# Optimization experiments

Hardware: AMD Instinct MI355X
Metric: run time of the kernel (lower is better)

## Reference

```python
import jax, jax.numpy as jnp
import numpy as np

N_NODES = 1_000_000
N_EDGES = 32_000_000
N_GRAPHS = 1024
N_LAYERS = 8


def setup_inputs() -> dict:
    key = jax.random.key(0)
    k1, k2, k3, k4, k5, k6, k7 = jax.random.split(key, 7)
    x = jnp.ones((N_NODES, 1), dtype=jnp.float32)
    src = jax.random.randint(k1, (N_EDGES,), 0, N_NODES, dtype=jnp.int32)
    dst = jax.random.randint(k2, (N_EDGES,), 0, N_NODES, dtype=jnp.int32)
    edge_weight = jax.random.uniform(k3, (N_EDGES,), dtype=jnp.float32)
    graph_ids = jnp.sort(jax.random.randint(k4, (N_NODES,), 0, N_GRAPHS, dtype=jnp.int32))
    W_neigh = jax.random.normal(k5, (N_LAYERS, 1, 1), dtype=jnp.float32)
    b_neigh = jax.random.normal(k6, (N_LAYERS, 1), dtype=jnp.float32)
    W_self = jax.random.normal(k7, (N_LAYERS, 1, 1), dtype=jnp.float32)
    return {"x": x, "src": src, "dst": dst, "edge_weight": edge_weight,
            "graph_ids": graph_ids, "W_neigh": W_neigh, "b_neigh": b_neigh,
            "W_self": W_self}


def reference(x, src, dst, edge_weight, graph_ids, W_neigh, b_neigh, W_self):
    # FixedNet forward with conv_type='GraphConvWL', concat_features=True.
    h = x
    xs = [h]
    for l in range(N_LAYERS):
        # GraphConv(norm='none'): sum over in-edges of src features * edge_weight,
        # then linear weight + bias.
        msg = h[src] * edge_weight[:, None]            # [E, 1]
        agg = jax.ops.segment_sum(msg, dst, num_segments=N_NODES)  # [N, 1]
        neigh = agg @ W_neigh[l] + b_neigh[l]          # conv_from_neigh
        self_f = h @ W_self[l]                          # conv_from_self (no bias)
        h = jax.nn.relu(neigh + self_f)
        xs.append(h)
    hcat = jnp.concatenate(xs, axis=1)                  # [N, N_LAYERS+1]
    # dgl.sum_nodes: per-graph sum over batched graphs
    hg = jax.ops.segment_sum(hcat, graph_ids, num_segments=N_GRAPHS)  # [G, 9]
    return hg
```

## Files before the change

kernel.cpp:

```cpp
#include <hip/hip_runtime.h>

#define N_NODES  1000000
#define N_EDGES  32000000
#define N_GRAPHS 1024
#define N_LAYERS 8
#define OUT_COLS (N_LAYERS + 1)

#define BKT_SHIFT 11
#define BKT_NODES 2048
#define NBKT      489
#define NBKT_PAD  512
#define SCAT_BLOCKS 256
#define SCAT_THREADS 1024
#define SCAT_CHUNK  (N_EDGES / SCAT_BLOCKS)

__device__ inline void seg_accum(int gid, float val, float* __restrict__ out, int col) {
    int g0 = __shfl(gid, 0);
    if (__all(gid == g0)) {
        #pragma unroll
        for (int off = 32; off > 0; off >>= 1)
            val += __shfl_down(val, off);
        if ((threadIdx.x & 63) == 0)
            atomicAdd(&out[g0 * OUT_COLS + col], val);
    } else {
        atomicAdd(&out[gid * OUT_COLS + col], val);
    }
}


__global__ void count_kernel(const int4* __restrict__ dst4, unsigned* __restrict__ g_count) {
    __shared__ unsigned hist[NBKT_PAD];
    for (int j = threadIdx.x; j < NBKT_PAD; j += blockDim.x) hist[j] = 0u;
    __syncthreads();
    int stride = gridDim.x * blockDim.x;
    for (int t = blockIdx.x * blockDim.x + threadIdx.x; t < N_EDGES / 4; t += stride) {
        int4 d = dst4[t];
        atomicAdd(&hist[((unsigned)d.x) >> BKT_SHIFT], 1u);
        atomicAdd(&hist[((unsigned)d.y) >> BKT_SHIFT], 1u);
        atomicAdd(&hist[((unsigned)d.z) >> BKT_SHIFT], 1u);
        atomicAdd(&hist[((unsigned)d.w) >> BKT_SHIFT], 1u);
    }
    __syncthreads();
    for (int j = threadIdx.x; j < NBKT_PAD; j += blockDim.x)
        if (hist[j]) atomicAdd(&g_count[j], hist[j]);
}

__global__ void scan_kernel(const unsigned* __restrict__ g_count,
                            unsigned* __restrict__ g_base,
                            unsigned* __restrict__ g_cursor) {
    __shared__ unsigned s[NBKT_PAD];
    int t = threadIdx.x;
    unsigned c = g_count[t];
    s[t] = c;
    __syncthreads();
    for (int off = 1; off < NBKT_PAD; off <<= 1) {
        unsigned v = (t >= off) ? s[t - off] : 0u;
        __syncthreads();
        s[t] += v;
        __syncthreads();
    }
    unsigned incl = s[t];
    g_base[t]   = incl - c;
    g_cursor[t] = incl - c;
    if (t == NBKT_PAD - 1) g_base[NBKT_PAD] = incl;
}

__global__ void scatter_kernel(const int* __restrict__ src,
                               const int* __restrict__ dst,
                               const float* __restrict__ ew,
                               unsigned* __restrict__ g_cursor,
                               unsigned long long* __restrict__ recs) {
    __shared__ unsigned lhist[NBKT_PAD];
    __shared__ unsigned lbase[NBKT_PAD];
    int e0 = blockIdx.x * SCAT_CHUNK;
    int e1 = e0 + SCAT_CHUNK;
    for (int j = threadIdx.x; j < NBKT_PAD; j += blockDim.x) lhist[j] = 0u;
    __syncthreads();
    for (int e = e0 + threadIdx.x; e < e1; e += blockDim.x)
        atomicAdd(&lhist[((unsigned)dst[e]) >> BKT_SHIFT], 1u);
    __syncthreads();
    for (int j = threadIdx.x; j < NBKT_PAD; j += blockDim.x) {
        unsigned c = lhist[j];
        lbase[j] = c ? atomicAdd(&g_cursor[j], c) : 0u;
    }
    __syncthreads();
    for (int j = threadIdx.x; j < NBKT_PAD; j += blockDim.x) lhist[j] = 0u;
    __syncthreads();
    for (int e = e0 + threadIdx.x; e < e1; e += blockDim.x) {
        unsigned d = (unsigned)dst[e];
        unsigned b = d >> BKT_SHIFT;
        unsigned loc = atomicAdd(&lhist[b], 1u);
        unsigned pos = lbase[b] + loc;
        unsigned hi  = ((unsigned)src[e]) | ((d & (BKT_NODES - 1u)) << 20);
        recs[pos] = ((unsigned long long)hi << 32) | (unsigned)__float_as_uint(ew[e]);
    }
}


__global__ void init_kernel(const float* __restrict__ x,
                            const int* __restrict__ gids,
                            float* __restrict__ h0,
                            float* __restrict__ out) {
    int i = blockIdx.x * blockDim.x + threadIdx.x;
    if (i >= N_NODES) return;
    float v = x[i];
    h0[i] = v;
    seg_accum(gids[i], v, out, 0);
}

__global__ void layer_kernel(const unsigned long long* __restrict__ recs,
                             const unsigned* __restrict__ g_base,
                             const float* __restrict__ h_old,
                             float* __restrict__ h_new,
                             const int* __restrict__ gids,
                             const float* __restrict__ Wn,
                             const float* __restrict__ bn,
                             const float* __restrict__ Ws,
                             float* __restrict__ out,
                             int l) {
    __shared__ float agg[BKT_NODES];
    int b = blockIdx.x;
    for (int j = threadIdx.x; j < BKT_NODES; j += blockDim.x) agg[j] = 0.0f;
    __syncthreads();
    int e0 = (int)g_base[b];
    int e1 = (int)g_base[b + 1];
    for (int e = e0 + threadIdx.x; e < e1; e += blockDim.x) {
        unsigned long long rec = __builtin_nontemporal_load(&recs[e]);
        unsigned hi = (unsigned)(rec >> 32);
        float w  = __uint_as_float((unsigned)rec);
        float hv = h_old[hi & 0xFFFFFu];
        atomicAdd(&agg[hi >> 20], hv * w);
    }
    __syncthreads();
    float wn = Wn[l], bb = bn[l], ws = Ws[l];
    int nbase = b << BKT_SHIFT;
    for (int j = threadIdx.x; j < BKT_NODES; j += blockDim.x) {
        int n = nbase + j;
        if (n < N_NODES) {
            float hn = fmaxf(fmaf(agg[j], wn, fmaf(h_old[n], ws, bb)), 0.0f);
            h_new[n] = hn;
            seg_accum(gids[n], hn, out, l + 1);
        }
    }
}


__global__ void fb_init_kernel(const float* __restrict__ x, const int* __restrict__ gids,
                               float* __restrict__ h, float* __restrict__ agg,
                               float* __restrict__ out) {
    int i = blockIdx.x * blockDim.x + threadIdx.x;
    if (i >= N_NODES) return;
    float v = x[i];
    h[i] = v; agg[i] = 0.0f;
    seg_accum(gids[i], v, out, 0);
}
__global__ void fb_edge_kernel(const int4* __restrict__ src4, const int4* __restrict__ dst4,
                               const float4* __restrict__ ew4, const float* __restrict__ h,
                               float* __restrict__ agg) {
    int t = blockIdx.x * blockDim.x + threadIdx.x;
    if (t >= N_EDGES / 4) return;
    int4 s = src4[t]; int4 d = dst4[t]; float4 w = ew4[t];
    atomicAdd(&agg[d.x], h[s.x] * w.x);
    atomicAdd(&agg[d.y], h[s.y] * w.y);
    atomicAdd(&agg[d.z], h[s.z] * w.z);
    atomicAdd(&agg[d.w], h[s.w] * w.w);
}
__global__ void fb_node_kernel(float* __restrict__ h, float* __restrict__ agg,
                               const int* __restrict__ gids, const float* __restrict__ Wn,
                               const float* __restrict__ bn, const float* __restrict__ Ws,
                               float* __restrict__ out, int l) {
    int i = blockIdx.x * blockDim.x + threadIdx.x;
    if (i >= N_NODES) return;
    float a = agg[i]; agg[i] = 0.0f;
    float hv = h[i];
    float hn = fmaxf(fmaf(a, Wn[l], fmaf(hv, Ws[l], bn[l])), 0.0f);
    h[i] = hn;
    seg_accum(gids[i], hn, out, l + 1);
}


extern "C" void kernel_launch(void* const* d_in, const int* in_sizes, int n_in,
                              void* d_out, int out_size, void* d_ws, size_t ws_size,
                              hipStream_t stream) {
    const float* x   = (const float*)d_in[0];
    const int*   src = (const int*)  d_in[1];
    const int*   dst = (const int*)  d_in[2];
    const float* ew  = (const float*)d_in[3];
    const int*   gid = (const int*)  d_in[4];
    const float* Wn  = (const float*)d_in[5];
    const float* bn  = (const float*)d_in[6];
    const float* Ws  = (const float*)d_in[7];
    float* out = (float*)d_out;

    hipMemsetAsync(d_out, 0, (size_t)out_size * sizeof(float), stream);

    size_t need = (size_t)N_EDGES * 8
                + (size_t)N_NODES * 4
                + (size_t)N_NODES * 4
                + (size_t)(NBKT_PAD * 3 + 16) * 4;

    if (ws_size < need) {
        float* h   = (float*)d_ws;
        float* agg = (float*)d_ws + N_NODES;
        const int BT = 256;
        const int nb = (N_NODES + BT - 1) / BT;
        const int eb = (N_EDGES / 4 + BT - 1) / BT;
        fb_init_kernel<<<nb, BT, 0, stream>>>(x, gid, h, agg, out);
        for (int l = 0; l < N_LAYERS; ++l) {
            fb_edge_kernel<<<eb, BT, 0, stream>>>(
                (const int4*)src, (const int4*)dst, (const float4*)ew, h, agg);
            fb_node_kernel<<<nb, BT, 0, stream>>>(h, agg, gid, Wn, bn, Ws, out, l);
        }
        return;
    }

    char* p = (char*)d_ws;
    unsigned long long* recs = (unsigned long long*)p;  p += (size_t)N_EDGES * 8;
    float*    h0       = (float*)p;                     p += (size_t)N_NODES * 4;
    float*    h1       = (float*)p;                     p += (size_t)N_NODES * 4;
    unsigned* g_count  = (unsigned*)p;                  p += NBKT_PAD * 4;
    unsigned* g_cursor = (unsigned*)p;                  p += NBKT_PAD * 4;
    unsigned* g_base   = (unsigned*)p;                  p += (NBKT_PAD + 1) * 4;

    hipMemsetAsync(g_count, 0, NBKT_PAD * 2 * sizeof(unsigned), stream);

    count_kernel  <<<2048, 256, 0, stream>>>((const int4*)dst, g_count);
    scan_kernel   <<<1, NBKT_PAD, 0, stream>>>(g_count, g_base, g_cursor);
    scatter_kernel<<<SCAT_BLOCKS, SCAT_THREADS, 0, stream>>>(src, dst, ew, g_cursor, recs);

    const int BT = 256;
    const int nb = (N_NODES + BT - 1) / BT;
    init_kernel<<<nb, BT, 0, stream>>>(x, gid, h0, out);

    float* ha = h0;
    float* hb = h1;
    for (int l = 0; l < N_LAYERS; ++l) {
        layer_kernel<<<NBKT, 512, 0, stream>>>(recs, g_base, ha, hb,
                                               gid, Wn, bn, Ws, out, l);
        float* t = ha; ha = hb; hb = t;
    }
}
```

Before: 2.266 ms.

## Split per-bucket edge aggregation across four blocks with separate node kernel

Each destination bucket's edge range is split over four blocks that each accumulate into shared memory and write a partial aggregate array, and a separate node kernel sums the four partials and applies the linear update, ReLU and per-graph accumulation. The edge loop is also unrolled by four so more gathers are in flight at once. This is meant to fix the low parallelism of 489 blocks on a GPU with many compute units. In exchange it adds a second launch per layer and extra global traffic for the partial arrays.

```diff
diff --git a/kernel.cpp b/kernel.cpp
--- a/kernel.cpp
+++ b/kernel.cpp
@@ -10,6 +10,7 @@
 #define BKT_NODES 2048
 #define NBKT      489
 #define NBKT_PAD  512
+#define KSPLIT    4
 #define SCAT_BLOCKS 256
 #define SCAT_THREADS 1024
 #define SCAT_CHUNK  (N_EDGES / SCAT_BLOCKS)
@@ -108,40 +109,66 @@
     seg_accum(gids[i], v, out, 0);
 }
 
-__global__ void layer_kernel(const unsigned long long* __restrict__ recs,
-                             const unsigned* __restrict__ g_base,
-                             const float* __restrict__ h_old,
-                             float* __restrict__ h_new,
-                             const int* __restrict__ gids,
-                             const float* __restrict__ Wn,
-                             const float* __restrict__ bn,
-                             const float* __restrict__ Ws,
-                             float* __restrict__ out,
-                             int l) {
+__global__ __launch_bounds__(512) void edge_kernel(
+        const unsigned long long* __restrict__ recs,
+        const unsigned* __restrict__ g_base,
+        const float* __restrict__ h_old,
+        float* __restrict__ partials) {
     __shared__ float agg[BKT_NODES];
-    int b = blockIdx.x;
-    for (int j = threadIdx.x; j < BKT_NODES; j += blockDim.x) agg[j] = 0.0f;
-    __syncthreads();
-    int e0 = (int)g_base[b];
-    int e1 = (int)g_base[b + 1];
-    for (int e = e0 + threadIdx.x; e < e1; e += blockDim.x) {
-        unsigned long long rec = __builtin_nontemporal_load(&recs[e]);
-        unsigned hi = (unsigned)(rec >> 32);
-        float w  = __uint_as_float((unsigned)rec);
-        float hv = h_old[hi & 0xFFFFFu];
-        atomicAdd(&agg[hi >> 20], hv * w);
-    }
-    __syncthreads();
-    float wn = Wn[l], bb = bn[l], ws = Ws[l];
-    int nbase = b << BKT_SHIFT;
-    for (int j = threadIdx.x; j < BKT_NODES; j += blockDim.x) {
-        int n = nbase + j;
-        if (n < N_NODES) {
-            float hn = fmaxf(fmaf(agg[j], wn, fmaf(h_old[n], ws, bb)), 0.0f);
-            h_new[n] = hn;
-            seg_accum(gids[n], hn, out, l + 1);
-        }
-    }
+    int blk = blockIdx.x;
+    int b   = blk >> 2;
+    int q   = blk & 3;
+    for (int j = threadIdx.x; j < BKT_NODES; j += 512) agg[j] = 0.0f;
+    __syncthreads();
+    int eb0 = (int)g_base[b];
+    int len = (int)g_base[b + 1] - eb0;
+    int qs  = eb0 + ((len * q) >> 2);
+    int qe  = eb0 + ((len * (q + 1)) >> 2);
+
+    int i = qs + threadIdx.x;
+    for (; i + 3 * 512 < qe; i += 4 * 512) {
+        unsigned long long r0 = __builtin_nontemporal_load(&recs[i]);
+        unsigned long long r1 = __builtin_nontemporal_load(&recs[i + 512]);
+        unsigned long long r2 = __builtin_nontemporal_load(&recs[i + 1024]);
+        unsigned long long r3 = __builtin_nontemporal_load(&recs[i + 1536]);
+        float h0v = h_old[(unsigned)(r0 >> 32) & 0xFFFFFu];
+        float h1v = h_old[(unsigned)(r1 >> 32) & 0xFFFFFu];
+        float h2v = h_old[(unsigned)(r2 >> 32) & 0xFFFFFu];
+        float h3v = h_old[(unsigned)(r3 >> 32) & 0xFFFFFu];
+        atomicAdd(&agg[(unsigned)(r0 >> 52)], h0v * __uint_as_float((unsigned)r0));
+        atomicAdd(&agg[(unsigned)(r1 >> 52)], h1v * __uint_as_float((unsigned)r1));
+        atomicAdd(&agg[(unsigned)(r2 >> 52)], h2v * __uint_as_float((unsigned)r2));
+        atomicAdd(&agg[(unsigned)(r3 >> 52)], h3v * __uint_as_float((unsigned)r3));
+    }
+    for (; i < qe; i += 512) {
+        unsigned long long r = __builtin_nontemporal_load(&recs[i]);
+        float hv = h_old[(unsigned)(r >> 32) & 0xFFFFFu];
+        atomicAdd(&agg[(unsigned)(r >> 52)], hv * __uint_as_float((unsigned)r));
+    }
+    __syncthreads();
+    float* pout = partials + (size_t)blk * BKT_NODES;
+    for (int j = threadIdx.x; j < BKT_NODES; j += 512)
+        pout[j] = agg[j];
+}
+
+__global__ void node_kernel(const float* __restrict__ partials,
+                            const float* __restrict__ h_old,
+                            float* __restrict__ h_new,
+                            const int* __restrict__ gids,
+                            const float* __restrict__ Wn,
+                            const float* __restrict__ bn,
+                            const float* __restrict__ Ws,
+                            float* __restrict__ out,
+                            int l) {
+    int n = blockIdx.x * blockDim.x + threadIdx.x;
+    if (n >= N_NODES) return;
+    int b = n >> BKT_SHIFT;
+    int j = n & (BKT_NODES - 1);
+    const float* p = partials + (size_t)(b * KSPLIT) * BKT_NODES + j;
+    float a = (p[0] + p[BKT_NODES]) + (p[2 * BKT_NODES] + p[3 * BKT_NODES]);
+    float hn = fmaxf(fmaf(a, Wn[l], fmaf(h_old[n], Ws[l], bn[l])), 0.0f);
+    h_new[n] = hn;
+    seg_accum(gids[n], hn, out, l + 1);
 }
 
 
@@ -195,8 +222,8 @@
     hipMemsetAsync(d_out, 0, (size_t)out_size * sizeof(float), stream);
 
     size_t need = (size_t)N_EDGES * 8
-                + (size_t)N_NODES * 4
-                + (size_t)N_NODES * 4
+                + (size_t)N_NODES * 4 * 2
+                + (size_t)NBKT * KSPLIT * BKT_NODES * 4
                 + (size_t)(NBKT_PAD * 3 + 16) * 4;
 
     if (ws_size < need) {
@@ -218,6 +245,7 @@
     unsigned long long* recs = (unsigned long long*)p;  p += (size_t)N_EDGES * 8;
     float*    h0       = (float*)p;                     p += (size_t)N_NODES * 4;
     float*    h1       = (float*)p;                     p += (size_t)N_NODES * 4;
+    float*    partials = (float*)p;                     p += (size_t)NBKT * KSPLIT * BKT_NODES * 4;
     unsigned* g_count  = (unsigned*)p;                  p += NBKT_PAD * 4;
     unsigned* g_cursor = (unsigned*)p;                  p += NBKT_PAD * 4;
     unsigned* g_base   = (unsigned*)p;                  p += (NBKT_PAD + 1) * 4;
@@ -235,8 +263,8 @@
     float* ha = h0;
     float* hb = h1;
     for (int l = 0; l < N_LAYERS; ++l) {
-        layer_kernel<<<NBKT, 512, 0, stream>>>(recs, g_base, ha, hb,
-                                               gid, Wn, bn, Ws, out, l);
+        edge_kernel<<<NBKT * KSPLIT, 512, 0, stream>>>(recs, g_base, ha, partials);
+        node_kernel<<<nb, BT, 0, stream>>>(partials, ha, hb, gid, Wn, bn, Ws, out, l);
         float* t = ha; ha = hb; hb = t;
     }
 }
```

After: 2.408 ms. +6.3%, slower.

## Sort bucketed edges into CSR by destination and use per-node pull layer

Applied to the files above, without the earlier changes.

Adds a per-bucket counting sort that reorders the bucketed edge records by exact destination node and builds a row pointer array. The layer kernel becomes a one-thread-per-node pull reduction with register accumulation, replacing shared-memory atomics. This requires a second 256MB record buffer and an extra sort pass, and per-thread sequential record reads are less coalesced across a wavefront. The previous bucket path is kept as a fallback when workspace is smaller.

```diff
diff --git a/kernel.cpp b/kernel.cpp
--- a/kernel.cpp
+++ b/kernel.cpp
@@ -96,6 +96,48 @@
     }
 }
 
+__global__ __launch_bounds__(1024) void sort_kernel(
+        const unsigned long long* __restrict__ recs_in,
+        const unsigned* __restrict__ g_base,
+        unsigned long long* __restrict__ recs_out,
+        unsigned* __restrict__ row_ptr) {
+    __shared__ unsigned cnt[BKT_NODES];
+    __shared__ unsigned ps[1024];
+    int b = blockIdx.x;
+    int t = threadIdx.x;
+    int e0 = (int)g_base[b];
+    int e1 = (int)g_base[b + 1];
+    cnt[t] = 0u; cnt[t + 1024] = 0u;
+    __syncthreads();
+    for (int e = e0 + t; e < e1; e += 1024)
+        atomicAdd(&cnt[(unsigned)(recs_in[e] >> 52)], 1u);
+    __syncthreads();
+    unsigned c0 = cnt[2 * t], c1 = cnt[2 * t + 1];
+    ps[t] = c0 + c1;
+    __syncthreads();
+    for (int off = 1; off < 1024; off <<= 1) {
+        unsigned u = (t >= off) ? ps[t - off] : 0u;
+        __syncthreads();
+        ps[t] += u;
+        __syncthreads();
+    }
+    unsigned exPair = ps[t] - (c0 + c1);
+    unsigned ex0 = exPair, ex1 = exPair + c0;
+    int nbase = b << BKT_SHIFT;
+    int n0 = nbase + 2 * t, n1 = n0 + 1;
+    if (n0 <= N_NODES) row_ptr[n0] = (unsigned)e0 + ex0;
+    if (n1 <= N_NODES) row_ptr[n1] = (unsigned)e0 + ex1;
+    __syncthreads();
+    cnt[2 * t] = ex0; cnt[2 * t + 1] = ex1;
+    __syncthreads();
+    for (int e = e0 + t; e < e1; e += 1024) {
+        unsigned long long r = recs_in[e];
+        unsigned j = (unsigned)(r >> 52);
+        unsigned pos = (unsigned)e0 + atomicAdd(&cnt[j], 1u);
+        recs_out[pos] = r;
+    }
+}
+
 
 __global__ void init_kernel(const float* __restrict__ x,
                             const int* __restrict__ gids,
@@ -108,16 +150,50 @@
     seg_accum(gids[i], v, out, 0);
 }
 
-__global__ void layer_kernel(const unsigned long long* __restrict__ recs,
-                             const unsigned* __restrict__ g_base,
-                             const float* __restrict__ h_old,
-                             float* __restrict__ h_new,
-                             const int* __restrict__ gids,
-                             const float* __restrict__ Wn,
-                             const float* __restrict__ bn,
-                             const float* __restrict__ Ws,
-                             float* __restrict__ out,
-                             int l) {
+__global__ __launch_bounds__(256) void layer_kernel(
+        const unsigned long long* __restrict__ recs,
+        const unsigned* __restrict__ row_ptr,
+        const float* __restrict__ h_old,
+        float* __restrict__ h_new,
+        const int* __restrict__ gids,
+        const float* __restrict__ Wn,
+        const float* __restrict__ bn,
+        const float* __restrict__ Ws,
+        float* __restrict__ out,
+        int l) {
+    int n = blockIdx.x * 256 + threadIdx.x;
+    if (n >= N_NODES) return;
+    int s = (int)row_ptr[n];
+    int e = (int)row_ptr[n + 1];
+    float a0 = 0.0f, a1 = 0.0f;
+    int i = s;
+    for (; i + 2 <= e; i += 2) {
+        unsigned long long r0 = recs[i];
+        unsigned long long r1 = recs[i + 1];
+        a0 = fmaf(h_old[(unsigned)(r0 >> 32) & 0xFFFFFu], __uint_as_float((unsigned)r0), a0);
+        a1 = fmaf(h_old[(unsigned)(r1 >> 32) & 0xFFFFFu], __uint_as_float((unsigned)r1), a1);
+    }
+    if (i < e) {
+        unsigned long long r0 = recs[i];
+        a0 = fmaf(h_old[(unsigned)(r0 >> 32) & 0xFFFFFu], __uint_as_float((unsigned)r0), a0);
+    }
+    float a = a0 + a1;
+    float hn = fmaxf(fmaf(a, Wn[l], fmaf(h_old[n], Ws[l], bn[l])), 0.0f);
+    h_new[n] = hn;
+    seg_accum(gids[n], hn, out, l + 1);
+}
+
+
+__global__ void bkt_layer_kernel(const unsigned long long* __restrict__ recs,
+                                 const unsigned* __restrict__ g_base,
+                                 const float* __restrict__ h_old,
+                                 float* __restrict__ h_new,
+                                 const int* __restrict__ gids,
+                                 const float* __restrict__ Wn,
+                                 const float* __restrict__ bn,
+                                 const float* __restrict__ Ws,
+                                 float* __restrict__ out,
+                                 int l) {
     __shared__ float agg[BKT_NODES];
     int b = blockIdx.x;
     for (int j = threadIdx.x; j < BKT_NODES; j += blockDim.x) agg[j] = 0.0f;
@@ -194,49 +270,81 @@
 
     hipMemsetAsync(d_out, 0, (size_t)out_size * sizeof(float), stream);
 
-    size_t need = (size_t)N_EDGES * 8
-                + (size_t)N_NODES * 4
-                + (size_t)N_NODES * 4
-                + (size_t)(NBKT_PAD * 3 + 16) * 4;
-
-    if (ws_size < need) {
-        float* h   = (float*)d_ws;
-        float* agg = (float*)d_ws + N_NODES;
-        const int BT = 256;
-        const int nb = (N_NODES + BT - 1) / BT;
-        const int eb = (N_EDGES / 4 + BT - 1) / BT;
-        fb_init_kernel<<<nb, BT, 0, stream>>>(x, gid, h, agg, out);
+    const int BT = 256;
+    const int nb = (N_NODES + BT - 1) / BT;
+
+    size_t need1 = (size_t)N_EDGES * 8 * 2
+                 + (size_t)(N_NODES + 2) * 4
+                 + (size_t)N_NODES * 4 * 2
+                 + (size_t)(NBKT_PAD * 3 + 16) * 4;
+    size_t need2 = (size_t)N_EDGES * 8
+                 + (size_t)N_NODES * 4 * 2
+                 + (size_t)(NBKT_PAD * 3 + 16) * 4;
+
+    if (ws_size >= need1) {
+        char* p = (char*)d_ws;
+        unsigned long long* recs_tmp = (unsigned long long*)p;  p += (size_t)N_EDGES * 8;
+        unsigned long long* recs     = (unsigned long long*)p;  p += (size_t)N_EDGES * 8;
+        unsigned* row_ptr  = (unsigned*)p;                      p += (size_t)(N_NODES + 2) * 4;
+        float*    h0       = (float*)p;                         p += (size_t)N_NODES * 4;
+        float*    h1       = (float*)p;                         p += (size_t)N_NODES * 4;
+        unsigned* g_count  = (unsigned*)p;                      p += NBKT_PAD * 4;
+        unsigned* g_cursor = (unsigned*)p;                      p += NBKT_PAD * 4;
+        unsigned* g_base   = (unsigned*)p;                      p += (NBKT_PAD + 1) * 4;
+
+        hipMemsetAsync(g_count, 0, NBKT_PAD * 2 * sizeof(unsigned), stream);
+
+        count_kernel  <<<2048, 256, 0, stream>>>((const int4*)dst, g_count);
+        scan_kernel   <<<1, NBKT_PAD, 0, stream>>>(g_count, g_base, g_cursor);
+        scatter_kernel<<<SCAT_BLOCKS, SCAT_THREADS, 0, stream>>>(src, dst, ew, g_cursor, recs_tmp);
+        sort_kernel   <<<NBKT, 1024, 0, stream>>>(recs_tmp, g_base, recs, row_ptr);
+
+        init_kernel<<<nb, BT, 0, stream>>>(x, gid, h0, out);
+
+        float* ha = h0;
+        float* hb = h1;
         for (int l = 0; l < N_LAYERS; ++l) {
-            fb_edge_kernel<<<eb, BT, 0, stream>>>(
-                (const int4*)src, (const int4*)dst, (const float4*)ew, h, agg);
-            fb_node_kernel<<<nb, BT, 0, stream>>>(h, agg, gid, Wn, bn, Ws, out, l);
+            layer_kernel<<<nb, BT, 0, stream>>>(recs, row_ptr, ha, hb,
+                                                gid, Wn, bn, Ws, out, l);
+            float* t = ha; ha = hb; hb = t;
         }
         return;
     }
 
-    char* p = (char*)d_ws;
-    unsigned long long* recs = (unsigned long long*)p;  p += (size_t)N_EDGES * 8;
-    float*    h0       = (float*)p;                     p += (size_t)N_NODES * 4;
-    float*    h1       = (float*)p;                     p += (size_t)N_NODES * 4;
-    unsigned* g_count  = (unsigned*)p;                  p += NBKT_PAD * 4;
-    unsigned* g_cursor = (unsigned*)p;                  p += NBKT_PAD * 4;
-    unsigned* g_base   = (unsigned*)p;                  p += (NBKT_PAD + 1) * 4;
-
-    hipMemsetAsync(g_count, 0, NBKT_PAD * 2 * sizeof(unsigned), stream);
-
-    count_kernel  <<<2048, 256, 0, stream>>>((const int4*)dst, g_count);
-    scan_kernel   <<<1, NBKT_PAD, 0, stream>>>(g_count, g_base, g_cursor);
-    scatter_kernel<<<SCAT_BLOCKS, SCAT_THREADS, 0, stream>>>(src, dst, ew, g_cursor, recs);
-
-    const int BT = 256;
-    const int nb = (N_NODES + BT - 1) / BT;
-    init_kernel<<<nb, BT, 0, stream>>>(x, gid, h0, out);
-
-    float* ha = h0;
-    float* hb = h1;
+    if (ws_size >= need2) {
+        char* p = (char*)d_ws;
+        unsigned long long* recs = (unsigned long long*)p;  p += (size_t)N_EDGES * 8;
+        float*    h0       = (float*)p;                     p += (size_t)N_NODES * 4;
+        float*    h1       = (float*)p;                     p += (size_t)N_NODES * 4;
+        unsigned* g_count  = (unsigned*)p;                  p += NBKT_PAD * 4;
+        unsigned* g_cursor = (unsigned*)p;                  p += NBKT_PAD * 4;
+        unsigned* g_base   = (unsigned*)p;                  p += (NBKT_PAD + 1) * 4;
+
+        hipMemsetAsync(g_count, 0, NBKT_PAD * 2 * sizeof(unsigned), stream);
+
+        count_kernel  <<<2048, 256, 0, stream>>>((const int4*)dst, g_count);
+        scan_kernel   <<<1, NBKT_PAD, 0, stream>>>(g_count, g_base, g_cursor);
+        scatter_kernel<<<SCAT_BLOCKS, SCAT_THREADS, 0, stream>>>(src, dst, ew, g_cursor, recs);
+
+        init_kernel<<<nb, BT, 0, stream>>>(x, gid, h0, out);
+
+        float* ha = h0;
+        float* hb = h1;
+        for (int l = 0; l < N_LAYERS; ++l) {
+            bkt_layer_kernel<<<NBKT, 512, 0, stream>>>(recs, g_base, ha, hb,
+                                                       gid, Wn, bn, Ws, out, l);
+            float* t = ha; ha = hb; hb = t;
+        }
+        return;
+    }
+
+    float* h   = (float*)d_ws;
+    float* agg = (float*)d_ws + N_NODES;
+    const int eb = (N_EDGES / 4 + BT - 1) / BT;
+    fb_init_kernel<<<nb, BT, 0, stream>>>(x, gid, h, agg, out);
     for (int l = 0; l < N_LAYERS; ++l) {
-        layer_kernel<<<NBKT, 512, 0, stream>>>(recs, g_base, ha, hb,
-                                               gid, Wn, bn, Ws, out, l);
-        float* t = ha; ha = hb; hb = t;
-    }
-}
+        fb_edge_kernel<<<eb, BT, 0, stream>>>(
+            (const int4*)src, (const int4*)dst, (const float4*)ew, h, agg);
+        fb_node_kernel<<<nb, BT, 0, stream>>>(h, agg, gid, Wn, bn, Ws, out, l);
+    }
+}
```

Measured after the change: 2.268 ms. About the same (+0.1%).
